# Kernel tuning notes

Hardware: AMD Instinct MI355X
Metric: run time of the kernel (lower is better)

Reference implementation:

```python
import jax, jax.numpy as jnp
import numpy as np
from jax import lax

B, T, D, H, L = 16, 256, 128, 128, 4  # batch, seq, input_size, hidden, num_layers
NUM_CLASSES = 10
EPS = 1e-5


def instancenorm(x):
    # x: [B, T, C]; InstanceNorm1d normalizes over the length dim (T) per (B, C),
    # biased variance, eps=1e-5, no affine.
    m = x.mean(axis=1, keepdims=True)
    v = x.var(axis=1, keepdims=True)
    return (x - m) / jnp.sqrt(v + EPS)


def lstm_stack(x, Wih, Whh, bih, bhh):
    # x: [B, T, I]; Wih/Whh: [L, 4H, I_or_H]; bih/bhh: [L, 4H]. Gate order i,f,g,o.
    batch = x.shape[0]
    hid = Whh.shape[-1]
    out = x
    for l in range(Wih.shape[0]):
        wih, whh, b = Wih[l], Whh[l], bih[l] + bhh[l]
        h0 = jnp.zeros((batch, hid), dtype=x.dtype)
        c0 = jnp.zeros((batch, hid), dtype=x.dtype)
        xs = out.swapaxes(0, 1)  # [T, B, I]

        def step(carry, xt):
            h, c = carry
            g = xt @ wih.T + h @ whh.T + b
            i, f, gg, o = jnp.split(g, 4, axis=-1)
            c_new = jax.nn.sigmoid(f) * c + jax.nn.sigmoid(i) * jnp.tanh(gg)
            h_new = jax.nn.sigmoid(o) * jnp.tanh(c_new)
            return (h_new, c_new), h_new

        _, hs = lax.scan(step, (h0, c0), xs)
        out = hs.swapaxes(0, 1)  # [B, T, H]
    return out


def setup_inputs() -> dict:
    key = jax.random.key(0)
    ks = jax.random.split(key, 16)
    s = 1.0 / np.sqrt(H)
    u = lambda k, shape: jax.random.uniform(k, shape, jnp.float32, -s, s)
    return {
        "x": jax.random.normal(ks[0], (B, T, D), jnp.float32),
        "Wih": u(ks[1], (L, 4 * H, D)),   # input_size == hidden_size so shapes stack
        "Whh": u(ks[2], (L, 4 * H, H)),
        "bih": u(ks[3], (L, 4 * H)),
        "bhh": u(ks[4], (L, 4 * H)),
        "proj_h_w": u(ks[5], (H, H)),
        "proj_h_b": u(ks[6], (H,)),
        "proj_x_w": u(ks[7], (H, D)),
        "proj_x_b": u(ks[8], (H,)),
        "attn_w": u(ks[9], (H,)),
        "fc_w": u(ks[10], (NUM_CLASSES, H)),
        "fc_b": u(ks[11], (NUM_CLASSES,)),
    }


def reference(x, Wih, Whh, bih, bhh, proj_h_w, proj_h_b, proj_x_w, proj_x_b, attn_w, fc_w, fc_b):
    batch, seq_len, input_dim = x.shape
    # normalize(): means/stdev are detached; torch std is unbiased (ddof=1)
    means = lax.stop_gradient(x.mean(axis=(0, 1), keepdims=True))
    stdev = lax.stop_gradient(x.std(axis=(0, 1), ddof=1, keepdims=True) + EPS)
    x = (x - means) / stdev
    x = instancenorm(x)

    lstm_out = lstm_stack(x, Wih, Whh, bih, bhh)   # dropout is identity in eval
    lstm_out = instancenorm(lstm_out)

    ph = lstm_out @ proj_h_w.T + proj_h_b           # [B, T, H]
    px = x @ proj_x_w.T + proj_x_b                  # [B, T, H]
    px = instancenorm(px)

    # additive attention over expanded [B, T, D, H] (values identical across D,
    # matching the original broadcast/expand semantics)
    combined = jnp.tanh(
        jnp.broadcast_to((ph + px)[:, :, None, :], (batch, seq_len, input_dim, ph.shape[-1]))
    )
    logits = jnp.einsum("btdh,h->btd", combined, attn_w)       # [B, T, D]
    alpha = jax.nn.softmax(logits.reshape(batch, -1), axis=1)   # softmax over T*D
    attention_map = alpha.reshape(batch, seq_len, input_dim)

    # classify: context = sum over (T, D) of lstm_out_ex * alpha
    context = jnp.einsum("bth,btd->bh", ph, attention_map)      # [B, H]
    out = context @ fc_w.T + fc_b                               # [B, num_classes]
    return out, attention_map
```

## Files before the change

### kernel.cpp

```cpp
#include <hip/hip_runtime.h>
#include <math.h>
#include <cstddef>

#define B_ 16
#define T_ 256
#define D_ 128
#define H_ 128
#define L_ 4
#define G_ 512
#define NC_ 10
#define EPS_ 1e-5f
#define C_ 16
#define NCHUNK_ (T_ / C_)

#define HROW_ 144
#define HOFF(k) ((k) + (((k) >> 5) << 2))

typedef float f4v __attribute__((ext_vector_type(4)));

#define LOAD_W8(w, base)                                                   \
    asm volatile(                                                          \
        "global_load_dwordx4 %0, %8, off\n\t"                             \
        "global_load_dwordx4 %1, %8, off offset:16\n\t"                   \
        "global_load_dwordx4 %2, %8, off offset:32\n\t"                   \
        "global_load_dwordx4 %3, %8, off offset:48\n\t"                   \
        "global_load_dwordx4 %4, %8, off offset:64\n\t"                   \
        "global_load_dwordx4 %5, %8, off offset:80\n\t"                   \
        "global_load_dwordx4 %6, %8, off offset:96\n\t"                   \
        "global_load_dwordx4 %7, %8, off offset:112\n\t"                  \
        "s_waitcnt vmcnt(0)"                                               \
        : "=&v"(w[0]), "=&v"(w[1]), "=&v"(w[2]), "=&v"(w[3]),              \
          "=&v"(w[4]), "=&v"(w[5]), "=&v"(w[6]), "=&v"(w[7])               \
        : "v"(base)                                                        \
        : "memory")

#define DOT32(dst_, warr_, hb_)                                            \
    {                                                                      \
        const f4v* h4_ = (const f4v*)(hb_);                                \
        float d0_ = 0.f, d1_ = 0.f;                                        \
        _Pragma("unroll")                                                  \
        for (int j_ = 0; j_ < 8; j_++) {                                   \
            f4v hv_ = h4_[j_];                                             \
            d0_ = fmaf(warr_[j_].x, hv_.x, d0_);                           \
            d1_ = fmaf(warr_[j_].y, hv_.y, d1_);                           \
            d0_ = fmaf(warr_[j_].z, hv_.z, d0_);                           \
            d1_ = fmaf(warr_[j_].w, hv_.w, d1_);                           \
        }                                                                  \
        dst_ = d0_ + d1_;                                                  \
    }

__device__ __forceinline__ float sigmoid_(float x) {
    x = fminf(fmaxf(x, -30.f), 30.f);
    return 1.f / (1.f + __expf(-x));
}
__device__ __forceinline__ float tanh_(float x) {
    float ax = fminf(fabsf(x), 15.f);
    float e = __expf(2.f * ax);
    float t = 1.f - 2.f / (e + 1.f);
    return copysignf(t, x);
}
__device__ __forceinline__ void wait_ge_(int* p, int v) {
    if (__hip_atomic_load(p, __ATOMIC_RELAXED, __HIP_MEMORY_SCOPE_AGENT) < v) {
        do { __builtin_amdgcn_s_sleep(1); }
        while (__hip_atomic_load(p, __ATOMIC_RELAXED, __HIP_MEMORY_SCOPE_AGENT) < v);
    }
    (void)__hip_atomic_load(p, __ATOMIC_ACQUIRE, __HIP_MEMORY_SCOPE_AGENT);
}

__global__ __launch_bounds__(512) void stats_bd(const float* __restrict__ x,
                                                float* __restrict__ sum_bd,
                                                float* __restrict__ sq_bd) {
    int b = blockIdx.x;
    int tid = threadIdx.x;
    int d = tid & 127, r = tid >> 7;
    const float* xb = x + (size_t)b * T_ * D_;
    float s = 0.f, q = 0.f;
    for (int t = r; t < T_; t += 4) {
        float v = xb[t * D_ + d];
        s += v; q += v * v;
    }
    __shared__ float ls[512], lq[512];
    ls[tid] = s; lq[tid] = q;
    __syncthreads();
    if (r == 0) {
        s = ls[d] + ls[d + 128] + ls[d + 256] + ls[d + 384];
        q = lq[d] + lq[d + 128] + lq[d + 256] + lq[d + 384];
        sum_bd[b * 128 + d] = s;
        sq_bd[b * 128 + d] = q;
    }
}

__global__ __launch_bounds__(128) void stats_d(const float* __restrict__ sum_bd,
                                               const float* __restrict__ sq_bd,
                                               float* __restrict__ sdv) {
    int d = threadIdx.x;
    float s = 0.f, q = 0.f;
    for (int b = 0; b < B_; b++) { s += sum_bd[b * 128 + d]; q += sq_bd[b * 128 + d]; }
    float n = (float)(B_ * T_);
    float m = s / n;
    float varu = (q - n * m * m) / (n - 1.f);
    varu = fmaxf(varu, 0.f);
    sdv[d] = sqrtf(varu) + EPS_;
}

__global__ __launch_bounds__(256) void normalize_x(const float* __restrict__ x,
                                                   const float* __restrict__ sum_bd,
                                                   const float* __restrict__ sq_bd,
                                                   const float* __restrict__ sdv,
                                                   float* __restrict__ xn) {
    int idx = blockIdx.x * 256 + threadIdx.x;
    int d = idx & 127;
    int b = idx >> 15;
    int bd = b * 128 + d;
    float mu = sum_bd[bd] * (1.f / T_);
    float varT = sq_bd[bd] * (1.f / T_) - mu * mu;
    float s = sdv[d];
    float inv = rsqrtf(fmaxf(varT, 0.f) + EPS_ * s * s);
    xn[idx] = (x[idx] - mu) * inv;
}

__global__ __launch_bounds__(256) void gemm_bias_k128(const float* __restrict__ A,
                                                      const float* __restrict__ Bw,
                                                      const float* __restrict__ b1,
                                                      const float* __restrict__ b2,
                                                      float* __restrict__ C, int N) {
    __shared__ __align__(16) float As[16][64];
    __shared__ __align__(16) float Bs[16][64];
    int tid = threadIdx.x;
    int m0 = blockIdx.x * 64, n0 = blockIdx.y * 64;
    int lr = tid >> 2;
    int lc = (tid & 3) << 2;
    int tm = (tid >> 4) << 2;
    int tn = (tid & 15) << 2;
    float acc[4][4] = {};
    const float* Arow = A + (size_t)(m0 + lr) * 128 + lc;
    const float* Brow = Bw + (size_t)(n0 + lr) * 128 + lc;
    for (int kb = 0; kb < 128; kb += 16) {
        float4 av = *(const float4*)(Arow + kb);
        float4 bv = *(const float4*)(Brow + kb);
        __syncthreads();
        As[lc + 0][lr] = av.x; As[lc + 1][lr] = av.y; As[lc + 2][lr] = av.z; As[lc + 3][lr] = av.w;
        Bs[lc + 0][lr] = bv.x; Bs[lc + 1][lr] = bv.y; Bs[lc + 2][lr] = bv.z; Bs[lc + 3][lr] = bv.w;
        __syncthreads();
#pragma unroll
        for (int k = 0; k < 16; k++) {
            float4 a4 = *(const float4*)&As[k][tm];
            float4 b4 = *(const float4*)&Bs[k][tn];
            float ar[4] = {a4.x, a4.y, a4.z, a4.w};
            float br[4] = {b4.x, b4.y, b4.z, b4.w};
#pragma unroll
            for (int i = 0; i < 4; i++)
#pragma unroll
                for (int j = 0; j < 4; j++)
                    acc[i][j] = fmaf(ar[i], br[j], acc[i][j]);
        }
    }
#pragma unroll
    for (int i = 0; i < 4; i++) {
        int row = m0 + tm + i;
#pragma unroll
        for (int j = 0; j < 4; j++) {
            int col = n0 + tn + j;
            float bias = b1[col] + (b2 ? b2[col] : 0.f);
            C[(size_t)row * N + col] = acc[i][j] + bias;
        }
    }
}

__global__ __attribute__((amdgpu_waves_per_eu(2, 2))) __launch_bounds__(512)
void scan_pipe4(const float* __restrict__ g0,
                const float* __restrict__ Wih, const float* __restrict__ Whh,
                const float* __restrict__ bih, const float* __restrict__ bhh,
                float* __restrict__ h_glob,
                float* __restrict__ ring,
                int* __restrict__ flag_h,
                int* __restrict__ flag_g) {
    const int wg = blockIdx.x;
    const int tid = threadIdx.x;
    const int r = tid >> 2, q = tid & 3;

    if (wg < 64) {
        const int l = wg >> 4, b = wg & 15;
        __shared__ __align__(16) float hsh[2][HROW_];
        f4v w0[8], w1[8], w2[8], w3[8];
        const float* wl = Whh + (size_t)l * G_ * 128;
        LOAD_W8(w0, wl + ((size_t)(0 * 128 + r)) * 128 + q * 32);
        LOAD_W8(w1, wl + ((size_t)(1 * 128 + r)) * 128 + q * 32);
        LOAD_W8(w2, wl + ((size_t)(2 * 128 + r)) * 128 + q * 32);
        LOAD_W8(w3, wl + ((size_t)(3 * 128 + r)) * 128 + q * 32);
        float c = 0.f;
        if (tid < HROW_) hsh[0][tid] = 0.f;
        const float* g0p = g0 + (size_t)b * T_ * G_;
        const float* rsl = (l > 0) ? ring + ((size_t)(l - 1) * 16 + b) * (4 * C_ * G_) : ring;
        float* hob = h_glob + ((size_t)l * 16 + b) * T_ * 128;
        int* fg = (l > 0) ? flag_g + (l - 1) * 16 + b : flag_g;
        int* fh = flag_h + l * 16 + b;
        float hreg[C_];
        __syncthreads();

        for (int k = 0; k < NCHUNK_; k++) {
            if (l > 0) {
                if (tid == 0) wait_ge_(fg, k + 1);
                __syncthreads();
            }
#pragma unroll
            for (int half = 0; half < 2; half++) {
                float p0[8], p1[8], p2[8], p3[8];
#pragma unroll
                for (int s8 = 0; s8 < 8; s8++) {
                    int s = half * 8 + s8;
                    if (l == 0) {
                        const float* gp = g0p + (size_t)(k * C_ + s) * G_;
                        p0[s8] = gp[r]; p1[s8] = gp[128 + r];
                        p2[s8] = gp[256 + r]; p3[s8] = gp[384 + r];
                    } else {
                        const float* gp = rsl + ((size_t)(k & 3) * C_ + s) * G_;
                        p0[s8] = __hip_atomic_load(gp + r, __ATOMIC_RELAXED, __HIP_MEMORY_SCOPE_AGENT);
                        p1[s8] = __hip_atomic_load(gp + 128 + r, __ATOMIC_RELAXED, __HIP_MEMORY_SCOPE_AGENT);
                        p2[s8] = __hip_atomic_load(gp + 256 + r, __ATOMIC_RELAXED, __HIP_MEMORY_SCOPE_AGENT);
                        p3[s8] = __hip_atomic_load(gp + 384 + r, __ATOMIC_RELAXED, __HIP_MEMORY_SCOPE_AGENT);
                    }
                }
#pragma unroll
                for (int s8 = 0; s8 < 8; s8++) {
                    int s = half * 8 + s8;
                    int t = k * C_ + s;
                    const float* hb = hsh[t & 1] + q * 36;
                    float zi, zf, zg, zo;
                    DOT32(zi, w0, hb);
                    DOT32(zf, w1, hb);
                    DOT32(zg, w2, hb);
                    DOT32(zo, w3, hb);
                    zi += __shfl_xor(zi, 1); zi += __shfl_xor(zi, 2);
                    zf += __shfl_xor(zf, 1); zf += __shfl_xor(zf, 2);
                    zg += __shfl_xor(zg, 1); zg += __shfl_xor(zg, 2);
                    zo += __shfl_xor(zo, 1); zo += __shfl_xor(zo, 2);
                    zi += p0[s8]; zf += p1[s8]; zg += p2[s8]; zo += p3[s8];
                    float ai = sigmoid_(zi), af = sigmoid_(zf);
                    float ag = tanh_(zg),    ao = sigmoid_(zo);
                    c = fmaf(af, c, ai * ag);
                    float hn = ao * tanh_(c);
                    if (q == 0) hsh[(t + 1) & 1][HOFF(r)] = hn;
                    hreg[s] = hn;
                    __syncthreads();
                }
            }
            if (q == 0) {
#pragma unroll
                for (int s = 0; s < C_; s++)
                    __hip_atomic_store(hob + (size_t)(k * C_ + s) * 128 + r, hreg[s],
                                       __ATOMIC_RELAXED, __HIP_MEMORY_SCOPE_AGENT);
            }
            __syncthreads();
            if (tid == 0) __hip_atomic_store(fh, k + 1, __ATOMIC_RELEASE, __HIP_MEMORY_SCOPE_AGENT);
        }
    } else {
        const int li = (wg - 64) >> 4;
        const int l = li + 1, b = (wg - 64) & 15;
        __shared__ __align__(16) float hch[C_][HROW_];
        f4v w0[8], w1[8], w2[8], w3[8];
        const float* wl = Wih + (size_t)l * G_ * 128;
        LOAD_W8(w0, wl + ((size_t)(0 * 128 + r)) * 128 + q * 32);
        LOAD_W8(w1, wl + ((size_t)(1 * 128 + r)) * 128 + q * 32);
        LOAD_W8(w2, wl + ((size_t)(2 * 128 + r)) * 128 + q * 32);
        LOAD_W8(w3, wl + ((size_t)(3 * 128 + r)) * 128 + q * 32);
        float bs0 = bih[l * G_ + r] + bhh[l * G_ + r];
        float bs1 = bih[l * G_ + 128 + r] + bhh[l * G_ + 128 + r];
        float bs2 = bih[l * G_ + 256 + r] + bhh[l * G_ + 256 + r];
        float bs3 = bih[l * G_ + 384 + r] + bhh[l * G_ + 384 + r];
        const float* hsrc = h_glob + ((size_t)(l - 1) * 16 + b) * T_ * 128;
        float* rout = ring + ((size_t)li * 16 + b) * (4 * C_ * G_);
        int* fhp = flag_h + (l - 1) * 16 + b;
        int* fhme = flag_h + l * 16 + b;
        int* fgo = flag_g + li * 16 + b;

        for (int k = 0; k < NCHUNK_; k++) {
            if (tid == 0) {
                wait_ge_(fhp, k + 1);
                if (k >= 4) wait_ge_(fhme, k - 3);
            }
            __syncthreads();
            {
#pragma unroll
                for (int i = 0; i < 4; i++) {
                    int idx = i * 512 + tid;
                    hch[idx >> 7][HOFF(idx & 127)] =
                        __hip_atomic_load(hsrc + (size_t)k * C_ * 128 + idx,
                                          __ATOMIC_RELAXED, __HIP_MEMORY_SCOPE_AGENT);
                }
            }
            __syncthreads();
#pragma unroll
            for (int s = 0; s < C_; s++) {
                const float* hb = hch[s] + q * 36;
                float z0, z1, z2, z3;
                DOT32(z0, w0, hb);
                DOT32(z1, w1, hb);
                DOT32(z2, w2, hb);
                DOT32(z3, w3, hb);
                z0 += __shfl_xor(z0, 1); z0 += __shfl_xor(z0, 2);
                z1 += __shfl_xor(z1, 1); z1 += __shfl_xor(z1, 2);
                z2 += __shfl_xor(z2, 1); z2 += __shfl_xor(z2, 2);
                z3 += __shfl_xor(z3, 1); z3 += __shfl_xor(z3, 2);
                if (q == 0) {
                    float* ro = rout + ((size_t)(k & 3) * C_ + s) * G_;
                    __hip_atomic_store(ro + r, z0 + bs0, __ATOMIC_RELAXED, __HIP_MEMORY_SCOPE_AGENT);
                    __hip_atomic_store(ro + 128 + r, z1 + bs1, __ATOMIC_RELAXED, __HIP_MEMORY_SCOPE_AGENT);
                    __hip_atomic_store(ro + 256 + r, z2 + bs2, __ATOMIC_RELAXED, __HIP_MEMORY_SCOPE_AGENT);
                    __hip_atomic_store(ro + 384 + r, z3 + bs3, __ATOMIC_RELAXED, __HIP_MEMORY_SCOPE_AGENT);
                }
            }
            __syncthreads();
            if (tid == 0) __hip_atomic_store(fgo, k + 1, __ATOMIC_RELEASE, __HIP_MEMORY_SCOPE_AGENT);
        }
    }
}

__global__ __launch_bounds__(512) void in_stats(const float* __restrict__ in,
                                                float* __restrict__ mu,
                                                float* __restrict__ inv) {
    int b = blockIdx.x;
    int tid = threadIdx.x;
    int h = tid & 127, r = tid >> 7;
    const float* ib = in + (size_t)b * T_ * H_;
    float s = 0.f, q = 0.f;
    for (int t = r; t < T_; t += 4) { float v = ib[t * H_ + h]; s += v; q += v * v; }
    __shared__ float ls[512], lq[512];
    ls[tid] = s; lq[tid] = q;
    __syncthreads();
    if (r == 0) {
        s = ls[h] + ls[h + 128] + ls[h + 256] + ls[h + 384];
        q = lq[h] + lq[h + 128] + lq[h + 256] + lq[h + 384];
        float m = s * (1.f / T_);
        float v = q * (1.f / T_) - m * m;
        mu[b * 128 + h] = m;
        inv[b * 128 + h] = rsqrtf(fmaxf(v, 0.f) + EPS_);
    }
}

__global__ __launch_bounds__(256) void apply_in(const float* __restrict__ in,
                                                const float* __restrict__ mu,
                                                const float* __restrict__ inv,
                                                float* __restrict__ out) {
    int idx = blockIdx.x * 256 + threadIdx.x;
    int h = idx & 127;
    int b = idx >> 15;
    out[idx] = (in[idx] - mu[b * 128 + h]) * inv[b * 128 + h];
}

__global__ __launch_bounds__(128) void score_kernel(const float* __restrict__ ph,
                                                    const float* __restrict__ px,
                                                    const float* __restrict__ mu_px,
                                                    const float* __restrict__ inv_px,
                                                    const float* __restrict__ attn_w,
                                                    float* __restrict__ lsc) {
    int bt = blockIdx.x;
    int b = bt >> 8;
    int h = threadIdx.x;
    size_t o = (size_t)bt * 128 + h;
    float v = ph[o] + (px[o] - mu_px[b * 128 + h]) * inv_px[b * 128 + h];
    float sv = tanh_(v) * attn_w[h];
    __shared__ float red[128];
    red[h] = sv;
    __syncthreads();
    for (int off = 64; off > 0; off >>= 1) {
        if (h < off) red[h] += red[h + off];
        __syncthreads();
    }
    if (h == 0) lsc[bt] = red[0];
}

__global__ __launch_bounds__(256) void softmax_t(const float* __restrict__ lsc,
                                                 float* __restrict__ wsm) {
    int b = blockIdx.x;
    int t = threadIdx.x;
    float v = lsc[b * 256 + t];
    __shared__ float red[256];
    red[t] = v; __syncthreads();
    for (int off = 128; off > 0; off >>= 1) { if (t < off) red[t] = fmaxf(red[t], red[t + off]); __syncthreads(); }
    float mx = red[0]; __syncthreads();
    float e = __expf(v - mx);
    red[t] = e; __syncthreads();
    for (int off = 128; off > 0; off >>= 1) { if (t < off) red[t] += red[t + off]; __syncthreads(); }
    wsm[b * 256 + t] = e / red[0];
}

__global__ __launch_bounds__(256) void att_map_write(const float* __restrict__ wsm,
                                                     float* __restrict__ out_att) {
    int idx = blockIdx.x * 256 + threadIdx.x;
    int b = idx >> 15;
    int t = (idx >> 7) & 255;
    out_att[idx] = wsm[b * 256 + t] * (1.f / (float)D_);
}

__global__ __launch_bounds__(128) void final_kernel(const float* __restrict__ ph,
                                                    const float* __restrict__ wsm,
                                                    const float* __restrict__ fc_w,
                                                    const float* __restrict__ fc_b,
                                                    float* __restrict__ out) {
    int b = blockIdx.x;
    int h = threadIdx.x;
    const float* pb = ph + (size_t)b * T_ * H_;
    const float* wb = wsm + b * 256;
    float acc = 0.f;
    for (int t = 0; t < T_; t++) acc = fmaf(pb[t * H_ + h], wb[t], acc);
    __shared__ float ctx[128];
    ctx[h] = acc;
    __syncthreads();
    if (h < NC_) {
        float s = fc_b[h];
        const float* fw = fc_w + h * 128;
        for (int k = 0; k < 128; k++) s = fmaf(ctx[k], fw[k], s);
        out[b * NC_ + h] = s;
    }
}

extern "C" void kernel_launch(void* const* d_in, const int* in_sizes, int n_in,
                              void* d_out, int out_size, void* d_ws, size_t ws_size,
                              hipStream_t stream) {
    const float* x        = (const float*)d_in[0];
    const float* Wih      = (const float*)d_in[1];
    const float* Whh      = (const float*)d_in[2];
    const float* bih      = (const float*)d_in[3];
    const float* bhh      = (const float*)d_in[4];
    const float* proj_h_w = (const float*)d_in[5];
    const float* proj_h_b = (const float*)d_in[6];
    const float* proj_x_w = (const float*)d_in[7];
    const float* proj_x_b = (const float*)d_in[8];
    const float* attn_w   = (const float*)d_in[9];
    const float* fc_w     = (const float*)d_in[10];
    const float* fc_b     = (const float*)d_in[11];
    float* out = (float*)d_out;

    float* ws = (float*)d_ws;
    const size_t NTD = (size_t)B_ * T_ * D_;
    float* xnorm  = ws;
    float* h_glob = xnorm + NTD;
    float* g0     = h_glob + 4 * NTD;
    float* ring   = g0 + 4 * NTD;
    float* smalls = ring + (size_t)3 * 16 * 4 * C_ * G_;
    float* sum_bd = smalls;
    float* sq_bd  = sum_bd + 2048;
    float* sdv    = sq_bd + 2048;
    float* mu_ln  = sdv + 128;
    float* inv_ln = mu_ln + 2048;
    float* mu_px  = inv_ln + 2048;
    float* inv_px = mu_px + 2048;
    float* lsc    = inv_px + 2048;
    float* wsm    = lsc + 4096;
    int*   flags  = (int*)(wsm + 4096);
    int*   flag_h = flags;
    int*   flag_g = flags + 64;
    float* lnorm = g0;
    float* ph    = h_glob;
    float* px    = h_glob + NTD;
    const float* h3 = h_glob + 3 * NTD;

    hipMemsetAsync((void*)flags, 0, 128 * sizeof(int), stream);

    stats_bd<<<16, 512, 0, stream>>>(x, sum_bd, sq_bd);
    stats_d<<<1, 128, 0, stream>>>(sum_bd, sq_bd, sdv);
    normalize_x<<<2048, 256, 0, stream>>>(x, sum_bd, sq_bd, sdv, xnorm);

    dim3 g1(64, 8);
    gemm_bias_k128<<<g1, 256, 0, stream>>>(xnorm, Wih, bih, bhh, g0, G_);
    scan_pipe4<<<112, 512, 0, stream>>>(g0, Wih, Whh, bih, bhh,
                                        h_glob, ring, flag_h, flag_g);

    in_stats<<<16, 512, 0, stream>>>(h3, mu_ln, inv_ln);
    apply_in<<<2048, 256, 0, stream>>>(h3, mu_ln, inv_ln, lnorm);
    dim3 g2(64, 2);
    gemm_bias_k128<<<g2, 256, 0, stream>>>(lnorm, proj_h_w, proj_h_b, nullptr, ph, H_);
    gemm_bias_k128<<<g2, 256, 0, stream>>>(xnorm, proj_x_w, proj_x_b, nullptr, px, H_);
    in_stats<<<16, 512, 0, stream>>>(px, mu_px, inv_px);

    score_kernel<<<4096, 128, 0, stream>>>(ph, px, mu_px, inv_px, attn_w, lsc);
    softmax_t<<<16, 256, 0, stream>>>(lsc, wsm);
    att_map_write<<<2048, 256, 0, stream>>>(wsm, out + B_ * NC_);
    final_kernel<<<16, 128, 0, stream>>>(ph, wsm, fc_w, fc_b, out);
}
```

Before: 520.6 us.

## Fuse instance-norm into projection GEMM and merge attention tail into one kernel

Folds the LSTM-output instance-norm apply step into the projection GEMM's A-tile load, which removes the apply_in kernel and its intermediate buffer. The px stats, score, softmax, attention-map write and final classifier kernels are merged into a single per-batch mega_tail kernel, cutting several launches and global round trips. The scan kernels now preload the h vector from shared memory into registers once per step and reuse it across the four gate dot products. The fused tail runs only 16 blocks, so its attention-map write and per-batch work get far less parallelism than the separate wide kernels had.

```diff
diff --git a/kernel.cpp b/kernel.cpp
--- a/kernel.cpp
+++ b/kernel.cpp
@@ -34,17 +34,15 @@
         : "v"(base)                                                        \
         : "memory")
 
-#define DOT32(dst_, warr_, hb_)                                            \
+#define DOT32R(dst_, warr_, hvarr_)                                        \
     {                                                                      \
-        const f4v* h4_ = (const f4v*)(hb_);                                \
         float d0_ = 0.f, d1_ = 0.f;                                        \
         _Pragma("unroll")                                                  \
         for (int j_ = 0; j_ < 8; j_++) {                                   \
-            f4v hv_ = h4_[j_];                                             \
-            d0_ = fmaf(warr_[j_].x, hv_.x, d0_);                           \
-            d1_ = fmaf(warr_[j_].y, hv_.y, d1_);                           \
-            d0_ = fmaf(warr_[j_].z, hv_.z, d0_);                           \
-            d1_ = fmaf(warr_[j_].w, hv_.w, d1_);                           \
+            d0_ = fmaf(warr_[j_].x, hvarr_[j_].x, d0_);                    \
+            d1_ = fmaf(warr_[j_].y, hvarr_[j_].y, d1_);                    \
+            d0_ = fmaf(warr_[j_].z, hvarr_[j_].z, d0_);                    \
+            d1_ = fmaf(warr_[j_].w, hvarr_[j_].w, d1_);                    \
         }                                                                  \
         dst_ = d0_ + d1_;                                                  \
     }
@@ -167,6 +165,61 @@
     }
 }
 
+__global__ __launch_bounds__(256) void gemm_norm_k128(const float* __restrict__ A,
+                                                      const float* __restrict__ mu,
+                                                      const float* __restrict__ inv,
+                                                      const float* __restrict__ Bw,
+                                                      const float* __restrict__ b1,
+                                                      float* __restrict__ C, int N) {
+    __shared__ __align__(16) float As[16][64];
+    __shared__ __align__(16) float Bs[16][64];
+    int tid = threadIdx.x;
+    int m0 = blockIdx.x * 64, n0 = blockIdx.y * 64;
+    int lr = tid >> 2;
+    int lc = (tid & 3) << 2;
+    int tm = (tid >> 4) << 2;
+    int tn = (tid & 15) << 2;
+    float acc[4][4] = {};
+    int bidx = (m0 + lr) >> 8;
+    const float* Arow = A + (size_t)(m0 + lr) * 128 + lc;
+    const float* Brow = Bw + (size_t)(n0 + lr) * 128 + lc;
+    const float* mup = mu + bidx * 128 + lc;
+    const float* ivp = inv + bidx * 128 + lc;
+    for (int kb = 0; kb < 128; kb += 16) {
+        float4 av = *(const float4*)(Arow + kb);
+        float4 m4 = *(const float4*)(mup + kb);
+        float4 i4 = *(const float4*)(ivp + kb);
+        av.x = (av.x - m4.x) * i4.x; av.y = (av.y - m4.y) * i4.y;
+        av.z = (av.z - m4.z) * i4.z; av.w = (av.w - m4.w) * i4.w;
+        float4 bv = *(const float4*)(Brow + kb);
+        __syncthreads();
+        As[lc + 0][lr] = av.x; As[lc + 1][lr] = av.y; As[lc + 2][lr] = av.z; As[lc + 3][lr] = av.w;
+        Bs[lc + 0][lr] = bv.x; Bs[lc + 1][lr] = bv.y; Bs[lc + 2][lr] = bv.z; Bs[lc + 3][lr] = bv.w;
+        __syncthreads();
+#pragma unroll
+        for (int k = 0; k < 16; k++) {
+            float4 a4 = *(const float4*)&As[k][tm];
+            float4 b4 = *(const float4*)&Bs[k][tn];
+            float ar[4] = {a4.x, a4.y, a4.z, a4.w};
+            float br[4] = {b4.x, b4.y, b4.z, b4.w};
+#pragma unroll
+            for (int i = 0; i < 4; i++)
+#pragma unroll
+                for (int j = 0; j < 4; j++)
+                    acc[i][j] = fmaf(ar[i], br[j], acc[i][j]);
+        }
+    }
+#pragma unroll
+    for (int i = 0; i < 4; i++) {
+        int row = m0 + tm + i;
+#pragma unroll
+        for (int j = 0; j < 4; j++) {
+            int col = n0 + tn + j;
+            C[(size_t)row * N + col] = acc[i][j] + b1[col];
+        }
+    }
+}
+
 __global__ __attribute__((amdgpu_waves_per_eu(2, 2))) __launch_bounds__(512)
 void scan_pipe4(const float* __restrict__ g0,
                 const float* __restrict__ Wih, const float* __restrict__ Whh,
@@ -225,12 +278,15 @@
                 for (int s8 = 0; s8 < 8; s8++) {
                     int s = half * 8 + s8;
                     int t = k * C_ + s;
-                    const float* hb = hsh[t & 1] + q * 36;
+                    const f4v* hb4 = (const f4v*)(hsh[t & 1] + q * 36);
+                    f4v hv[8];
+#pragma unroll
+                    for (int j = 0; j < 8; j++) hv[j] = hb4[j];
                     float zi, zf, zg, zo;
-                    DOT32(zi, w0, hb);
-                    DOT32(zf, w1, hb);
-                    DOT32(zg, w2, hb);
-                    DOT32(zo, w3, hb);
+                    DOT32R(zi, w0, hv);
+                    DOT32R(zf, w1, hv);
+                    DOT32R(zg, w2, hv);
+                    DOT32R(zo, w3, hv);
                     zi += __shfl_xor(zi, 1); zi += __shfl_xor(zi, 2);
                     zf += __shfl_xor(zf, 1); zf += __shfl_xor(zf, 2);
                     zg += __shfl_xor(zg, 1); zg += __shfl_xor(zg, 2);
@@ -292,12 +348,15 @@
             __syncthreads();
 #pragma unroll
             for (int s = 0; s < C_; s++) {
-                const float* hb = hch[s] + q * 36;
+                const f4v* hb4 = (const f4v*)(hch[s] + q * 36);
+                f4v hv[8];
+#pragma unroll
+                for (int j = 0; j < 8; j++) hv[j] = hb4[j];
                 float z0, z1, z2, z3;
-                DOT32(z0, w0, hb);
-                DOT32(z1, w1, hb);
-                DOT32(z2, w2, hb);
-                DOT32(z3, w3, hb);
+                DOT32R(z0, w0, hv);
+                DOT32R(z1, w1, hv);
+                DOT32R(z2, w2, hv);
+                DOT32R(z3, w3, hv);
                 z0 += __shfl_xor(z0, 1); z0 += __shfl_xor(z0, 2);
                 z1 += __shfl_xor(z1, 1); z1 += __shfl_xor(z1, 2);
                 z2 += __shfl_xor(z2, 1); z2 += __shfl_xor(z2, 2);
@@ -338,80 +397,76 @@
     }
 }
 
-__global__ __launch_bounds__(256) void apply_in(const float* __restrict__ in,
-                                                const float* __restrict__ mu,
-                                                const float* __restrict__ inv,
-                                                float* __restrict__ out) {
-    int idx = blockIdx.x * 256 + threadIdx.x;
-    int h = idx & 127;
-    int b = idx >> 15;
-    out[idx] = (in[idx] - mu[b * 128 + h]) * inv[b * 128 + h];
-}
-
-__global__ __launch_bounds__(128) void score_kernel(const float* __restrict__ ph,
-                                                    const float* __restrict__ px,
-                                                    const float* __restrict__ mu_px,
-                                                    const float* __restrict__ inv_px,
-                                                    const float* __restrict__ attn_w,
-                                                    float* __restrict__ lsc) {
-    int bt = blockIdx.x;
-    int b = bt >> 8;
-    int h = threadIdx.x;
-    size_t o = (size_t)bt * 128 + h;
-    float v = ph[o] + (px[o] - mu_px[b * 128 + h]) * inv_px[b * 128 + h];
-    float sv = tanh_(v) * attn_w[h];
-    __shared__ float red[128];
-    red[h] = sv;
+__global__ __launch_bounds__(256) void mega_tail(const float* __restrict__ ph,
+                                                 const float* __restrict__ px,
+                                                 const float* __restrict__ attn_w,
+                                                 const float* __restrict__ fc_w,
+                                                 const float* __restrict__ fc_b,
+                                                 float* __restrict__ out,
+                                                 float* __restrict__ out_att) {
+    int b = blockIdx.x;
+    int tid = threadIdx.x;
+    int h = tid & 127, st = tid >> 7;
+    int wv = tid >> 6, ln = tid & 63;
+    const float* pxb = px + (size_t)b * T_ * H_;
+    const float* phb = ph + (size_t)b * T_ * H_;
+    __shared__ float muS[128], invS[128];
+    __shared__ float ls[256], lq[256];
+    __shared__ float lsc[256], tmp[256], wsh[256];
+
+    {
+        float s = 0.f, q = 0.f;
+        for (int t = st; t < T_; t += 2) { float v = pxb[t * 128 + h]; s += v; q += v * v; }
+        ls[tid] = s; lq[tid] = q;
+        __syncthreads();
+        if (st == 0) {
+            s = ls[h] + ls[h + 128]; q = lq[h] + lq[h + 128];
+            float m = s * (1.f / T_);
+            float v = q * (1.f / T_) - m * m;
+            muS[h] = m;
+            invS[h] = rsqrtf(fmaxf(v, 0.f) + EPS_);
+        }
+        __syncthreads();
+    }
+    for (int t4 = 0; t4 < T_; t4 += 4) {
+        int t = t4 + wv;
+        float v0 = phb[t * 128 + ln] + (pxb[t * 128 + ln] - muS[ln]) * invS[ln];
+        float v1 = phb[t * 128 + 64 + ln] + (pxb[t * 128 + 64 + ln] - muS[64 + ln]) * invS[64 + ln];
+        float sv = tanh_(v0) * attn_w[ln] + tanh_(v1) * attn_w[64 + ln];
+#pragma unroll
+        for (int off = 32; off > 0; off >>= 1) sv += __shfl_down(sv, off);
+        if (ln == 0) lsc[t] = sv;
+    }
     __syncthreads();
-    for (int off = 64; off > 0; off >>= 1) {
-        if (h < off) red[h] += red[h + off];
-        __syncthreads();
-    }
-    if (h == 0) lsc[bt] = red[0];
-}
-
-__global__ __launch_bounds__(256) void softmax_t(const float* __restrict__ lsc,
-                                                 float* __restrict__ wsm) {
-    int b = blockIdx.x;
-    int t = threadIdx.x;
-    float v = lsc[b * 256 + t];
-    __shared__ float red[256];
-    red[t] = v; __syncthreads();
-    for (int off = 128; off > 0; off >>= 1) { if (t < off) red[t] = fmaxf(red[t], red[t + off]); __syncthreads(); }
-    float mx = red[0]; __syncthreads();
-    float e = __expf(v - mx);
-    red[t] = e; __syncthreads();
-    for (int off = 128; off > 0; off >>= 1) { if (t < off) red[t] += red[t + off]; __syncthreads(); }
-    wsm[b * 256 + t] = e / red[0];
-}
-
-__global__ __launch_bounds__(256) void att_map_write(const float* __restrict__ wsm,
-                                                     float* __restrict__ out_att) {
-    int idx = blockIdx.x * 256 + threadIdx.x;
-    int b = idx >> 15;
-    int t = (idx >> 7) & 255;
-    out_att[idx] = wsm[b * 256 + t] * (1.f / (float)D_);
-}
-
-__global__ __launch_bounds__(128) void final_kernel(const float* __restrict__ ph,
-                                                    const float* __restrict__ wsm,
-                                                    const float* __restrict__ fc_w,
-                                                    const float* __restrict__ fc_b,
-                                                    float* __restrict__ out) {
-    int b = blockIdx.x;
-    int h = threadIdx.x;
-    const float* pb = ph + (size_t)b * T_ * H_;
-    const float* wb = wsm + b * 256;
-    float acc = 0.f;
-    for (int t = 0; t < T_; t++) acc = fmaf(pb[t * H_ + h], wb[t], acc);
-    __shared__ float ctx[128];
-    ctx[h] = acc;
-    __syncthreads();
-    if (h < NC_) {
-        float s = fc_b[h];
-        const float* fw = fc_w + h * 128;
-        for (int k = 0; k < 128; k++) s = fmaf(ctx[k], fw[k], s);
-        out[b * NC_ + h] = s;
+    {
+        float v = lsc[tid];
+        tmp[tid] = v; __syncthreads();
+        for (int off = 128; off > 0; off >>= 1) { if (tid < off) tmp[tid] = fmaxf(tmp[tid], tmp[tid + off]); __syncthreads(); }
+        float mx = tmp[0]; __syncthreads();
+        float e = __expf(v - mx);
+        tmp[tid] = e; __syncthreads();
+        for (int off = 128; off > 0; off >>= 1) { if (tid < off) tmp[tid] += tmp[tid + off]; __syncthreads(); }
+        wsh[tid] = e / tmp[0];
+        __syncthreads();
+    }
+    {
+        float* ob = out_att + (size_t)b * T_ * D_;
+        const float invD = 1.f / (float)D_;
+        for (int i = tid; i < T_ * D_; i += 256) ob[i] = wsh[i >> 7] * invD;
+    }
+    {
+        float acc = 0.f;
+        for (int t = st; t < T_; t += 2) acc = fmaf(phb[t * 128 + h], wsh[t], acc);
+        ls[tid] = acc;
+        __syncthreads();
+        if (tid < 128) ls[tid] = ls[tid] + ls[tid + 128];
+        __syncthreads();
+        if (tid < NC_) {
+            float s = fc_b[tid];
+            const float* fw = fc_w + tid * 128;
+            for (int k = 0; k < 128; k++) s = fmaf(ls[k], fw[k], s);
+            out[b * NC_ + tid] = s;
+        }
     }
 }
 
@@ -444,14 +499,9 @@
     float* sdv    = sq_bd + 2048;
     float* mu_ln  = sdv + 128;
     float* inv_ln = mu_ln + 2048;
-    float* mu_px  = inv_ln + 2048;
-    float* inv_px = mu_px + 2048;
-    float* lsc    = inv_px + 2048;
-    float* wsm    = lsc + 4096;
-    int*   flags  = (int*)(wsm + 4096);
+    int*   flags  = (int*)(inv_ln + 2048);
     int*   flag_h = flags;
     int*   flag_g = flags + 64;
-    float* lnorm = g0;
     float* ph    = h_glob;
     float* px    = h_glob + NTD;
     const float* h3 = h_glob + 3 * NTD;
@@ -468,14 +518,9 @@
                                         h_glob, ring, flag_h, flag_g);
 
     in_stats<<<16, 512, 0, stream>>>(h3, mu_ln, inv_ln);
-    apply_in<<<2048, 256, 0, stream>>>(h3, mu_ln, inv_ln, lnorm);
     dim3 g2(64, 2);
-    gemm_bias_k128<<<g2, 256, 0, stream>>>(lnorm, proj_h_w, proj_h_b, nullptr, ph, H_);
+    gemm_norm_k128<<<g2, 256, 0, stream>>>(h3, mu_ln, inv_ln, proj_h_w, proj_h_b, ph, H_);
     gemm_bias_k128<<<g2, 256, 0, stream>>>(xnorm, proj_x_w, proj_x_b, nullptr, px, H_);
-    in_stats<<<16, 512, 0, stream>>>(px, mu_px, inv_px);
-
-    score_kernel<<<4096, 128, 0, stream>>>(ph, px, mu_px, inv_px, attn_w, lsc);
-    softmax_t<<<16, 256, 0, stream>>>(lsc, wsm);
-    att_map_write<<<2048, 256, 0, stream>>>(wsm, out + B_ * NC_);
-    final_kernel<<<16, 128, 0, stream>>>(ph, wsm, fc_w, fc_b, out);
-}
+
+    mega_tail<<<16, 256, 0, stream>>>(ph, px, attn_w, fc_w, fc_b, out, out + B_ * NC_);
+}
```

Measured after the change: 562.3 us. 8.0% more time.
